# Kernel tuning notes

Hardware: AMD Instinct MI355X
Metric: run time of the kernel (lower is better)

The kernel has to match this reference:

```python
import jax, jax.numpy as jnp
import numpy as np
from jax import lax

VOCAB = 32000
N_E = 1024
N_D = 1024
DEPTH = 4
L = 512
B = 8
HIGHWAY_BIAS = -3.0  # args.bias, folded into forget-gate bias


def setup_inputs() -> dict:
    key = jax.random.key(0)
    ks = jax.random.split(key, 8)
    x = jax.random.randint(ks[0], (L, B), 0, VOCAB)
    hidden = jnp.zeros((DEPTH, B, N_D), dtype=jnp.float32)
    emb = jax.random.normal(ks[1], (VOCAB, N_E), dtype=jnp.float32) * (3.0 / VOCAB) ** 0.5
    W0 = jax.random.normal(ks[2], (N_E, 4 * N_D), dtype=jnp.float32) * N_E ** -0.5
    Wl = jax.random.normal(ks[3], (DEPTH - 1, N_D, 3 * N_D), dtype=jnp.float32) * N_D ** -0.5
    vc = jax.random.normal(ks[4], (DEPTH, 2 * N_D), dtype=jnp.float32) * 0.1
    out_W = jax.random.normal(ks[5], (N_D, VOCAB), dtype=jnp.float32) * (3.0 / VOCAB) ** 0.5
    out_b = jnp.zeros((VOCAB,), dtype=jnp.float32)
    return {"x": x, "hidden": hidden, "emb": emb, "W0": W0, "Wl": Wl,
            "vc": vc, "out_W": out_W, "out_b": out_b}


def _sru_layer(u0, u1, u2, resid, vf, vr, c0):
    # u*: (L, B, d) precomputed GEMM outputs; scan only does elementwise recurrence.
    def step(c, inp):
        u0t, u1t, u2t, rt = inp
        f = jax.nn.sigmoid(u1t + vf * c + HIGHWAY_BIAS)
        r = jax.nn.sigmoid(u2t + vr * c)
        c_new = f * c + (1.0 - f) * u0t
        h = r * c_new + (1.0 - r) * rt
        return c_new, h
    c_last, hs = lax.scan(step, c0, (u0, u1, u2, resid))
    return hs, c_last


def reference(x, hidden, emb, W0, Wl, vc, out_W, out_b):
    h = emb[x]  # (L, B, n_e); dropout disabled (p=0)
    c_finals = []
    for layer in range(DEPTH):
        if layer == 0:
            U = jnp.einsum('lbe,ek->lbk', h, W0).reshape(L, B, 4, N_D)
            resid = U[:, :, 3]  # k=4: transformed input as highway residual
        else:
            U = jnp.einsum('lbd,dk->lbk', h, Wl[layer - 1]).reshape(L, B, 3, N_D)
            resid = h           # k=3: highway residual is the layer input
        vf = vc[layer, :N_D]
        vr = vc[layer, N_D:]
        h, c_last = _sru_layer(U[:, :, 0], U[:, :, 1], U[:, :, 2], resid, vf, vr, hidden[layer])
        c_finals.append(c_last)
    out = h.reshape(L * B, N_D) @ out_W + out_b  # (L*B, vocab)
    return out, jnp.stack(c_finals)
```

## Files before the change

kernel.cpp:

```cpp
#include <hip/hip_runtime.h>
#include <hip/hip_bf16.h>

#define L_SEQ 512
#define BATCH 8
#define ND 1024
#define VOCAB_N 32000
#define MROWS 4096
#define KDIM 1024
#define NKS 32
#define NSCAN 128

typedef unsigned short u16;
typedef unsigned int u32;
using bf16x8 = __attribute__((ext_vector_type(8))) __bf16;
using f32x4  = __attribute__((ext_vector_type(4))) float;
using u16x8  = __attribute__((ext_vector_type(8))) unsigned short;
using u16x4  = __attribute__((ext_vector_type(4))) unsigned short;

#define BAR() asm volatile("s_barrier" ::: "memory")
#define VMW(n) asm volatile("s_waitcnt vmcnt(" #n ")" ::: "memory")
#define LGKM0() asm volatile("s_waitcnt lgkmcnt(0)" ::: "memory")
#define SCHED() __builtin_amdgcn_sched_barrier(0)

static __device__ __forceinline__ u16 f2bf(float f) {
  u32 u = __builtin_bit_cast(u32, f);
  u32 r = u + 0x7FFF + ((u >> 16) & 1);
  return (u16)(r >> 16);
}
static __device__ __forceinline__ float bf2f(u16 b) {
  u32 u = ((u32)b) << 16;
  return __builtin_bit_cast(float, u);
}
static __device__ __forceinline__ void gload16(const void* g, void* l) {
  __builtin_amdgcn_global_load_lds(
      (const __attribute__((address_space(1))) void*)g,
      (__attribute__((address_space(3))) void*)l, 16, 0, 0);
}

static __device__ __forceinline__ void transpose_body(int tb, const float* __restrict__ W,
                                                      u16* __restrict__ Wt, int Ndim) {
  __shared__ float s[32][33];
  int nx = Ndim >> 5;
  int n0 = (tb % nx) * 32, k0 = (tb / nx) * 32;
  int tid = threadIdx.x;
  int tx = tid & 31, ty = tid >> 5;
#pragma unroll
  for (int i = 0; i < 4; i++)
    s[ty * 4 + i][tx] = __builtin_nontemporal_load(
        &W[(size_t)(k0 + ty * 4 + i) * Ndim + n0 + tx]);
  __syncthreads();
  int n = tid >> 3, kg = tid & 7;
  u16x4 o;
#pragma unroll
  for (int j = 0; j < 4; j++) o[j] = f2bf(s[kg * 4 + j][n]);
  *(u16x4*)(Wt + (size_t)(n0 + n) * KDIM + k0 + kg * 4) = o;
}

__global__ __launch_bounds__(256) void k_embed_t(const int* __restrict__ x,
                                                 const float* __restrict__ emb,
                                                 u16* __restrict__ h,
                                                 const float* __restrict__ Wsrc,
                                                 u16* __restrict__ WtOut, int NdimT) {
  if (blockIdx.x >= 2048) {
    transpose_body(blockIdx.x - 2048, Wsrc, WtOut, NdimT);
    return;
  }
  int t = blockIdx.x * 256 + threadIdx.x;
  int fidx = t * 8;
  int row = fidx >> 10;
  int col = fidx & 1023;
  int tok = x[row];
  const float4* src = (const float4*)(emb + (size_t)tok * ND + col);
  float4 a = src[0], b = src[1];
  u16x8 o;
  o[0]=f2bf(a.x); o[1]=f2bf(a.y); o[2]=f2bf(a.z); o[3]=f2bf(a.w);
  o[4]=f2bf(b.x); o[5]=f2bf(b.y); o[6]=f2bf(b.z); o[7]=f2bf(b.w);
  *(u16x8*)(h + fidx) = o;
}

__global__ __launch_bounds__(256) void k_transpose_cast(const float* __restrict__ W,
                                                        u16* __restrict__ Wt, int Ndim) {
  transpose_body(blockIdx.x, W, Wt, Ndim);
}

static __device__ __forceinline__ bf16x8 frag32(const char* smbase, int r, int cb) {
  int p = r * 64 + cb;
  p ^= ((p >> 7) & 3) << 4;
  return *(const bf16x8*)(smbase + p);
}

__global__ __launch_bounds__(512, 4) void k_gemm_out(const u16* __restrict__ A,
                                                     const u16* __restrict__ Bt,
                                                     float* __restrict__ CoutF, int Ndim,
                                                     const float* __restrict__ bias) {
  extern __shared__ __align__(16) char sm[];

  int bid = blockIdx.x;
  int xcd = bid & 7;
  int i = bid >> 3;
  int bm = (xcd << 2) | (i & 3);
  int bn = i >> 2;
  int m0 = bm * 128, n0 = bn * 256;

  int tid = threadIdx.x;
  int lane = tid & 63, w = tid >> 6;
  int wm = w >> 2, wn = w & 3;
  int l15 = lane & 15, hi16 = lane >> 4;

  f32x4 acc[4][4] = {};
  bf16x8 aA[4], bB[4];

  const u16* Ab = A + (size_t)m0 * KDIM;
  const u16* Bb = Bt + (size_t)n0 * KDIM;

  auto stage = [&](int t, int base) {
    {
      int d = tid * 16;
      int o = d ^ (((d >> 7) & 3) << 4);
      gload16(Ab + (size_t)(o >> 6) * KDIM + t * 32 + ((o & 63) >> 1), sm + base + d);
    }
#pragma unroll
    for (int j = 0; j < 2; ++j) {
      int d = (j * 512 + tid) * 16;
      int o = d ^ (((d >> 7) & 3) << 4);
      gload16(Bb + (size_t)(o >> 6) * KDIM + t * 32 + ((o & 63) >> 1),
              sm + base + 8192 + d);
    }
  };

  stage(0, 0);
  stage(1, 24576);
  VMW(3);
  BAR();

  const int cb = hi16 * 16;
  const int ra = wm * 64 + l15;
  const int rbv = wn * 64 + l15;

#pragma unroll 1
  for (int t = 0; t < NKS; ++t) {
    const bool st = (t + 2 < NKS);
    const int cur = (t & 1) * 24576;
#pragma unroll
    for (int mi = 0; mi < 4; ++mi) aA[mi] = frag32(sm + cur, ra + mi * 16, cb);
#pragma unroll
    for (int ni = 0; ni < 4; ++ni) bB[ni] = frag32(sm + cur + 8192, rbv + ni * 16, cb);
    LGKM0();
    SCHED();
    BAR();
    if (st) stage(t + 2, cur);
    __builtin_amdgcn_s_setprio(1);
#pragma unroll
    for (int mi = 0; mi < 4; ++mi)
#pragma unroll
      for (int ni = 0; ni < 4; ++ni)
        acc[mi][ni] = __builtin_amdgcn_mfma_f32_16x16x32_bf16(aA[mi], bB[ni], acc[mi][ni], 0, 0, 0);
    __builtin_amdgcn_s_setprio(0);
    SCHED();
    if (st) { VMW(3); } else { VMW(0); }
    BAR();
  }

  float* epi = (float*)sm;
  for (int p = 0; p < 4; ++p) {
    if (p) __syncthreads();
    if (wn == p) {
#pragma unroll
      for (int mi = 0; mi < 4; ++mi)
#pragma unroll
        for (int ni = 0; ni < 4; ++ni)
#pragma unroll
          for (int r = 0; r < 4; ++r)
            epi[(wm * 64 + mi * 16 + hi16 * 4 + r) * 68 + ni * 16 + l15] = acc[mi][ni][r];
    }
    __syncthreads();
    int gcolbase = n0 + p * 64;
#pragma unroll
    for (int i2 = 0; i2 < 4; ++i2) {
      int fidx = i2 * 2048 + tid * 4;
      int row = fidx >> 6, col = fidx & 63;
      f32x4 v = *(const f32x4*)(epi + row * 68 + col);
      int gcol = gcolbase + col;
      const float4 bb = *(const float4*)(bias + gcol);
      v[0] += bb.x; v[1] += bb.y; v[2] += bb.z; v[3] += bb.w;
      __builtin_nontemporal_store(v, (f32x4*)(CoutF + (size_t)(m0 + row) * Ndim + gcol));
    }
  }
}

template <int EPI>
__global__ __launch_bounds__(256, 3) void k_gemm128(const u16* __restrict__ A,
                                                    const u16* __restrict__ Bt,
                                                    u16* __restrict__ Cout, int Ndim) {
  extern __shared__ __align__(16) char sm[];

  int bid = blockIdx.x;
  int xcd = bid & 7;
  int i = bid >> 3;
  int bm = (xcd << 2) | (i & 3);
  int bn = i >> 2;
  int m0 = bm * 128, n0 = bn * 128;

  int tid = threadIdx.x;
  int lane = tid & 63, w = tid >> 6;
  int wm = w >> 1, wn = w & 1;
  int l15 = lane & 15, hi16 = lane >> 4;

  f32x4 acc[4][4] = {};
  bf16x8 aA[4], bB[4];

  const u16* Ab = A + (size_t)m0 * KDIM;
  const u16* Bb = Bt + (size_t)n0 * KDIM;

  auto stage = [&](int t, int base) {
#pragma unroll
    for (int j = 0; j < 2; ++j) {
      int d = (j * 256 + tid) * 16;
      int o = d ^ (((d >> 7) & 3) << 4);
      gload16(Ab + (size_t)(o >> 6) * KDIM + t * 32 + ((o & 63) >> 1), sm + base + d);
    }
#pragma unroll
    for (int j = 0; j < 2; ++j) {
      int d = (j * 256 + tid) * 16;
      int o = d ^ (((d >> 7) & 3) << 4);
      gload16(Bb + (size_t)(o >> 6) * KDIM + t * 32 + ((o & 63) >> 1),
              sm + base + 8192 + d);
    }
  };

  stage(0, 0);
  stage(1, 16384);
  VMW(4);
  BAR();

  const int cb = hi16 * 16;
  const int ra = wm * 64 + l15;
  const int rbv = wn * 64 + l15;

  int rb = 0, sb = 2;
#pragma unroll 1
  for (int t = 0; t < NKS; ++t) {
    const bool st = (t + 2 < NKS);
    if (st) stage(t + 2, sb * 16384);
    const char* cur = sm + rb * 16384;
#pragma unroll
    for (int mi = 0; mi < 4; ++mi) aA[mi] = frag32(cur, ra + mi * 16, cb);
#pragma unroll
    for (int ni = 0; ni < 4; ++ni) bB[ni] = frag32(cur + 8192, rbv + ni * 16, cb);
    __builtin_amdgcn_s_setprio(1);
#pragma unroll
    for (int mi = 0; mi < 4; ++mi)
#pragma unroll
      for (int ni = 0; ni < 4; ++ni)
        acc[mi][ni] = __builtin_amdgcn_mfma_f32_16x16x32_bf16(aA[mi], bB[ni], acc[mi][ni], 0, 0, 0);
    __builtin_amdgcn_s_setprio(0);
    SCHED();
    if (st) { VMW(4); } else { VMW(0); }
    BAR();
    rb = (rb == 2) ? 0 : rb + 1;
    sb = (sb == 2) ? 0 : sb + 1;
  }

  float* epi = (float*)sm;
  for (int p = 0; p < 2; ++p) {
    if (p) __syncthreads();
    if (wn == p) {
#pragma unroll
      for (int mi = 0; mi < 4; ++mi)
#pragma unroll
        for (int ni = 0; ni < 4; ++ni)
#pragma unroll
          for (int r = 0; r < 4; ++r)
            epi[(wm * 64 + mi * 16 + hi16 * 4 + r) * 68 + ni * 16 + l15] = acc[mi][ni][r];
    }
    __syncthreads();
    int gcolbase = n0 + p * 64;
    int plane = gcolbase >> 10;
#pragma unroll
    for (int i2 = 0; i2 < 8; ++i2) {
      int fidx = i2 * 1024 + tid * 4;
      int row = fidx >> 6, col = fidx & 63;
      f32x4 v = *(const f32x4*)(epi + row * 68 + col);
      int gcol = gcolbase + col;
      if (plane == 1) {
#pragma unroll
        for (int j = 0; j < 4; j++) v[j] = -1.44269504f * (v[j] - 3.0f);
      } else if (plane == 2) {
#pragma unroll
        for (int j = 0; j < 4; j++) v[j] = -1.44269504f * v[j];
      }
      u16x4 o;
#pragma unroll
      for (int j = 0; j < 4; j++) o[j] = f2bf(v[j]);
      *(u16x4*)(Cout + (size_t)(m0 + row) * Ndim + gcol) = o;
    }
  }
}

__global__ __launch_bounds__(256) void k_scan(const u16* __restrict__ U, int P,
                                              const u16* __restrict__ resid, int rstride,
                                              u16* __restrict__ hout,
                                              const float* __restrict__ vc,
                                              const float* __restrict__ hidden,
                                              float* __restrict__ cfin, int layer,
                                              const float* __restrict__ Wsrc,
                                              u16* __restrict__ WtOut, int NdimT) {
  if (blockIdx.x >= NSCAN) {
    transpose_body(blockIdx.x - NSCAN, Wsrc, WtOut, NdimT);
    return;
  }
  if (threadIdx.x >= 64) return;
  int cid = blockIdx.x * 64 + threadIdx.x;
  int b = cid >> 10, d = cid & 1023;
  float vfp = -1.44269504f * vc[layer * 2048 + d];
  float vrp = -1.44269504f * vc[layer * 2048 + 1024 + d];
  float c = hidden[layer * 8192 + cid];
  const u16* pu = U + (size_t)b * P * 1024 + d;
  const u16* pr = resid + (size_t)b * rstride + d;
  u16* ph = hout + (size_t)b * 1024 + d;
  const int ustep = P * 1024;
  const int rstep = rstride;

  u16 su0[16], sa1[16], sa2[16], srs[16];
#pragma unroll
  for (int j = 0; j < 16; j++) {
    su0[j] = pu[(size_t)(8 * j) * ustep];
    sa1[j] = pu[(size_t)(8 * j) * ustep + 1024];
    sa2[j] = pu[(size_t)(8 * j) * ustep + 2048];
    srs[j] = pr[(size_t)(8 * j) * rstep];
  }
  for (int tb = 0; tb < L_SEQ; tb += 16) {
#pragma unroll
    for (int j = 0; j < 16; j++) {
      int t = tb + j;
      float u0f = bf2f(su0[j]), a1f = bf2f(sa1[j]);
      float a2f = bf2f(sa2[j]), rf = bf2f(srs[j]);
      int tp = (t + 16) & 511;
      su0[j] = pu[(size_t)(8 * tp) * ustep];
      sa1[j] = pu[(size_t)(8 * tp) * ustep + 1024];
      sa2[j] = pu[(size_t)(8 * tp) * ustep + 2048];
      srs[j] = pr[(size_t)(8 * tp) * rstep];
      float e1 = __builtin_amdgcn_exp2f(fmaf(vfp, c, a1f));
      float e2 = __builtin_amdgcn_exp2f(fmaf(vrp, c, a2f));
      float fv = __builtin_amdgcn_rcpf(1.0f + e1);
      float rv = __builtin_amdgcn_rcpf(1.0f + e2);
      float cn = fmaf(fv, c - u0f, u0f);
      float hv = fmaf(rv, cn - rf, rf);
      ph[(size_t)t * (BATCH * ND)] = f2bf(hv);
      c = cn;
    }
  }
  cfin[layer * 8192 + cid] = c;
}

extern "C" void kernel_launch(void* const* d_in, const int* in_sizes, int n_in,
                              void* d_out, int out_size, void* d_ws, size_t ws_size,
                              hipStream_t stream) {
  const int*   x      = (const int*)d_in[0];
  const float* hidden = (const float*)d_in[1];
  const float* emb    = (const float*)d_in[2];
  const float* W0     = (const float*)d_in[3];
  const float* Wl     = (const float*)d_in[4];
  const float* vc     = (const float*)d_in[5];
  const float* outW   = (const float*)d_in[6];
  const float* outb   = (const float*)d_in[7];
  float* out = (float*)d_out;

  char* ws = (char*)d_ws;
  u16* hA    = (u16*)ws;
  u16* hB    = (u16*)(ws + 8388608);
  u16* U     = (u16*)(ws + 16777216);
  u16* Wt    = (u16*)(ws + 50331648);
  float* cfin = out + (size_t)MROWS * VOCAB_N;

  const size_t wtbig_off_big = 58720256;
  bool bigws = ws_size >= (size_t)(wtbig_off_big + (size_t)VOCAB_N * KDIM * 2);
  u16* WtBig = (u16*)(ws + (bigws ? wtbig_off_big : 16777216));

  k_embed_t<<<2048 + 4096, 256, 0, stream>>>(x, emb, hA, W0, Wt, 4096);

  k_gemm128<0><<<32 * 32, 256, 49152, stream>>>(hA, Wt, U, 4096);
  k_scan<<<NSCAN + 3072, 256, 0, stream>>>(U, 4, U + 3 * 1024, 4 * 1024, hB, vc, hidden,
                                           cfin, 0, Wl, Wt, 3072);

  const u16* hin[3]  = {hB, hA, hB};
  u16*       hout[3] = {hA, hB, hA};
  for (int l = 1; l <= 3; l++) {
    k_gemm128<1><<<32 * 24, 256, 49152, stream>>>(hin[l - 1], Wt, U, 3072);
    if (l < 3) {
      k_scan<<<NSCAN + 3072, 256, 0, stream>>>(U, 3, hin[l - 1], 1024, hout[l - 1], vc,
                                               hidden, cfin, l,
                                               Wl + (size_t)l * KDIM * 3072, Wt, 3072);
    } else if (bigws) {
      k_scan<<<NSCAN + 32000, 256, 0, stream>>>(U, 3, hin[l - 1], 1024, hout[l - 1], vc,
                                                hidden, cfin, l, outW, WtBig, VOCAB_N);
    } else {
      k_scan<<<NSCAN, 256, 0, stream>>>(U, 3, hin[l - 1], 1024, hout[l - 1], vc,
                                        hidden, cfin, l, nullptr, nullptr, 32);
      k_transpose_cast<<<32000, 256, 0, stream>>>(outW, WtBig, VOCAB_N);
    }
  }

  k_gemm_out<<<32 * 125, 512, 49152, stream>>>(hA, WtBig, out, VOCAB_N, outb);
}
```

Measured before the change: 660.4 us.

## Pack final hidden states in MFMA fragment order and load A directly from global

```diff
diff --git a/kernel.cpp b/kernel.cpp
--- a/kernel.cpp
+++ b/kernel.cpp
@@ -110,45 +110,41 @@
   f32x4 acc[4][4] = {};
   bf16x8 aA[4], bB[4];
 
-  const u16* Ab = A + (size_t)m0 * KDIM;
   const u16* Bb = Bt + (size_t)n0 * KDIM;
-
-  auto stage = [&](int t, int base) {
-    {
-      int d = tid * 16;
-      int o = d ^ (((d >> 7) & 3) << 4);
-      gload16(Ab + (size_t)(o >> 6) * KDIM + t * 32 + ((o & 63) >> 1), sm + base + d);
-    }
+  const int mbBase = bm * 8 + wm * 4;
+  const u16* Apl = A + lane * 8;
+
+  auto stageB = [&](int t, int base) {
 #pragma unroll
     for (int j = 0; j < 2; ++j) {
       int d = (j * 512 + tid) * 16;
       int o = d ^ (((d >> 7) & 3) << 4);
       gload16(Bb + (size_t)(o >> 6) * KDIM + t * 32 + ((o & 63) >> 1),
-              sm + base + 8192 + d);
+              sm + base + d);
     }
   };
 
-  stage(0, 0);
-  stage(1, 24576);
-  VMW(3);
+  stageB(0, 0);
+  stageB(1, 16384);
+  VMW(2);
   BAR();
 
   const int cb = hi16 * 16;
-  const int ra = wm * 64 + l15;
   const int rbv = wn * 64 + l15;
 
 #pragma unroll 1
   for (int t = 0; t < NKS; ++t) {
     const bool st = (t + 2 < NKS);
-    const int cur = (t & 1) * 24576;
-#pragma unroll
-    for (int mi = 0; mi < 4; ++mi) aA[mi] = frag32(sm + cur, ra + mi * 16, cb);
-#pragma unroll
-    for (int ni = 0; ni < 4; ++ni) bB[ni] = frag32(sm + cur + 8192, rbv + ni * 16, cb);
+    const int cur = (t & 1) * 16384;
+#pragma unroll
+    for (int mi = 0; mi < 4; ++mi)
+      aA[mi] = *(const bf16x8*)(Apl + ((size_t)((mbBase + mi) * 32 + t) << 9));
+#pragma unroll
+    for (int ni = 0; ni < 4; ++ni) bB[ni] = frag32(sm + cur, rbv + ni * 16, cb);
     LGKM0();
     SCHED();
     BAR();
-    if (st) stage(t + 2, cur);
+    if (st) stageB(t + 2, cur);
     __builtin_amdgcn_s_setprio(1);
 #pragma unroll
     for (int mi = 0; mi < 4; ++mi)
@@ -157,7 +153,7 @@
         acc[mi][ni] = __builtin_amdgcn_mfma_f32_16x16x32_bf16(aA[mi], bB[ni], acc[mi][ni], 0, 0, 0);
     __builtin_amdgcn_s_setprio(0);
     SCHED();
-    if (st) { VMW(3); } else { VMW(0); }
+    if (st) { VMW(2); } else { VMW(0); }
     BAR();
   }
 
@@ -318,6 +314,8 @@
   const u16* pu = U + (size_t)b * P * 1024 + d;
   const u16* pr = resid + (size_t)b * rstride + d;
   u16* ph = hout + (size_t)b * 1024 + d;
+  u16* pp = hout + ((d >> 5) * 512 + ((d >> 3) & 3) * 128 + b * 8 + (d & 7));
+  const bool pack = (layer == 3);
   const int ustep = P * 1024;
   const int rstep = rstride;
 
@@ -346,7 +344,9 @@
       float rv = __builtin_amdgcn_rcpf(1.0f + e2);
       float cn = fmaf(fv, c - u0f, u0f);
       float hv = fmaf(rv, cn - rf, rf);
-      ph[(size_t)t * (BATCH * ND)] = f2bf(hv);
+      u16 hb = f2bf(hv);
+      if (pack) pp[(t >> 1) * 16384 + (t & 1) * 64] = hb;
+      else      ph[(size_t)t * (BATCH * ND)] = hb;
       c = cn;
     }
   }
@@ -401,5 +401,5 @@
     }
   }
 
-  k_gemm_out<<<32 * 125, 512, 49152, stream>>>(hA, WtBig, out, VOCAB_N, outb);
-}
+  k_gemm_out<<<32 * 125, 512, 34816, stream>>>(hA, WtBig, out, VOCAB_N, outb);
+}
```

Measured after the change: 722.8 us. 1.09x slower.
